# Performance work log

Hardware: AMD Instinct MI355X
Metric: run time of the kernel (lower is better)

Reference implementation:

```python
import jax, jax.numpy as jnp
import numpy as np

D_MODEL = 768
NUM_HEADS = 12
DEPTH = D_MODEL // NUM_HEADS


def setup_inputs() -> dict:
    key = jax.random.key(0)
    ks = jax.random.split(key, 11)
    B, S, D = 2, 2048, D_MODEL
    scale = 1.0 / np.sqrt(D)
    inp = {
        "v": jax.random.normal(ks[0], (B, S, D), jnp.float32),
        "k": jax.random.normal(ks[1], (B, S, D), jnp.float32),
        "q": jax.random.normal(ks[2], (B, S, D), jnp.float32),
        "wq": jax.random.normal(ks[3], (D, D), jnp.float32) * scale,
        "bq": jnp.zeros((D,), jnp.float32),
        "wk": jax.random.normal(ks[4], (D, D), jnp.float32) * scale,
        "bk": jnp.zeros((D,), jnp.float32),
        "wv": jax.random.normal(ks[5], (D, D), jnp.float32) * scale,
        "bv": jnp.zeros((D,), jnp.float32),
        "wo": jax.random.normal(ks[6], (D, D), jnp.float32) * scale,
        "bo": jnp.zeros((D,), jnp.float32),
    }
    return inp


def _split_heads(x):
    # (B, S, D) -> (B, H, S, depth)
    B, S, _ = x.shape
    return x.reshape(B, S, NUM_HEADS, DEPTH).transpose(0, 2, 1, 3)


def reference(v, k, q, wq, bq, wk, bk, wv, bv, wo, bo):
    B, S, D = q.shape
    qh = _split_heads(q @ wq + bq)  # (B,H,S,dh)
    kh = _split_heads(k @ wk + bk)
    vh = _split_heads(v @ wv + bv)
    logits = jnp.einsum("bhqd,bhkd->bhqk", qh, kh) / jnp.sqrt(
        jnp.asarray(DEPTH, qh.dtype)
    )
    attn = jax.nn.softmax(logits, axis=-1)  # (B,H,S,S)
    ctx = jnp.einsum("bhqk,bhkd->bhqd", attn, vh)
    ctx = ctx.transpose(0, 2, 1, 3).reshape(B, S, D)
    return ctx @ wo + bo
```

## Files before the change

kernel.cpp:

```cpp
#include <hip/hip_runtime.h>
#include <hip/hip_bf16.h>
#include <math.h>

typedef __bf16 bf16;
typedef __attribute__((ext_vector_type(8))) __bf16 bf16x8;
typedef __attribute__((ext_vector_type(4))) __bf16 bf16x4v;
typedef __attribute__((ext_vector_type(4))) float f32x4;

#define MFMA16(a, b, c) __builtin_amdgcn_mfma_f32_16x16x32_bf16(a, b, c, 0, 0, 0)

__device__ __forceinline__ void gld16(const bf16* g, bf16* l) {
  __builtin_amdgcn_global_load_lds((const __attribute__((address_space(1))) void*)g,
                                   (__attribute__((address_space(3))) void*)l, 16, 0, 0);
}

__global__ __launch_bounds__(256) void prep(const float* __restrict__ q,
                                            const float* __restrict__ k,
                                            const float* __restrict__ v,
                                            bf16* __restrict__ qb, bf16* __restrict__ kb,
                                            bf16* __restrict__ vb,
                                            const float* __restrict__ w0,
                                            const float* __restrict__ w1,
                                            const float* __restrict__ w2,
                                            const float* __restrict__ w3,
                                            bf16* __restrict__ t0, bf16* __restrict__ t1,
                                            bf16* __restrict__ t2, bf16* __restrict__ t3) {
  const int lin = blockIdx.x;
  if (lin < 4608) {
    const int which = lin / 1536, idx = lin % 1536;
    const float* a = which == 0 ? q : (which == 1 ? k : v);
    bf16* o = which == 0 ? qb : (which == 1 ? kb : vb);
    const size_t i = ((size_t)idx * 256 + threadIdx.x) * 8;
    const float4 f0 = *(const float4*)(a + i);
    const float4 f1 = *(const float4*)(a + i + 4);
    bf16x8 r = {(bf16)f0.x, (bf16)f0.y, (bf16)f0.z, (bf16)f0.w,
                (bf16)f1.x, (bf16)f1.y, (bf16)f1.z, (bf16)f1.w};
    *(bf16x8*)(o + i) = r;
  } else {
    const int w = lin - 4608;
    const int z = w / 576, rem = w % 576;
    const int by = rem / 24, bx = rem % 24;
    const float* W = z == 0 ? w0 : (z == 1 ? w1 : (z == 2 ? w2 : w3));
    bf16* T = z == 0 ? t0 : (z == 1 ? t1 : (z == 2 ? t2 : t3));
    __shared__ float t[32][33];
    const int tx = threadIdx.x & 31, ty = threadIdx.x >> 5;
    const int c0 = bx * 32, r0 = by * 32;
#pragma unroll
    for (int i = 0; i < 4; ++i) {
      const int r = ty + 8 * i;
      t[r][tx] = W[(size_t)(r0 + r) * 768 + c0 + tx];
    }
    __syncthreads();
#pragma unroll
    for (int i = 0; i < 4; ++i) {
      const int r = ty + 8 * i;
      T[(size_t)(c0 + r) * 768 + r0 + tx] = (bf16)t[tx][r];
    }
  }
}

__device__ __forceinline__ void gemm_core(const bf16* __restrict__ A, const bf16* __restrict__ BT,
                                          int row0, int col0, bf16* As, bf16* Bs,
                                          f32x4 acc[4][4]) {
  const int tid = threadIdx.x;
  const int lane = tid & 63, wave = tid >> 6;
  const int m15 = lane & 15, kg = lane >> 4;
  const int wm = wave >> 1, wn = wave & 1;
  const int pr16 = lane & 15;
  const int pk8 = (lane >> 4) * 8;
#pragma unroll
  for (int i = 0; i < 4; ++i)
#pragma unroll
    for (int j = 0; j < 4; ++j) acc[i][j] = f32x4{0.f, 0.f, 0.f, 0.f};

  for (int k0 = 0; k0 < 768; k0 += 32) {
#pragma unroll
    for (int j = 0; j < 2; ++j) {
      const int i = wave * 2 + j;
      gld16(A + (size_t)(row0 + 16 * i + pr16) * 768 + k0 + pk8, As + i * 512);
      gld16(BT + (size_t)(col0 + 16 * i + pr16) * 768 + k0 + pk8, Bs + i * 512);
    }
    __syncthreads();
    bf16x8 af[4], bfr[4];
#pragma unroll
    for (int t = 0; t < 4; ++t)
      af[t] = *(const bf16x8*)(As + (4 * wm + t) * 512 + kg * 128 + m15 * 8);
#pragma unroll
    for (int t = 0; t < 4; ++t)
      bfr[t] = *(const bf16x8*)(Bs + (4 * wn + t) * 512 + kg * 128 + m15 * 8);
#pragma unroll
    for (int mt = 0; mt < 4; ++mt)
#pragma unroll
      for (int nt = 0; nt < 4; ++nt) acc[mt][nt] = MFMA16(af[mt], bfr[nt], acc[mt][nt]);
    __syncthreads();
  }
}

__global__ __launch_bounds__(256, 3) void gemm_qkv(
    const bf16* __restrict__ qb, const bf16* __restrict__ kb, const bf16* __restrict__ vb,
    const bf16* __restrict__ wqT, const bf16* __restrict__ wkT, const bf16* __restrict__ wvT,
    const float* __restrict__ bq, const float* __restrict__ bk, const float* __restrict__ bv,
    bf16* __restrict__ Qh, bf16* __restrict__ Kh, bf16* __restrict__ Vt) {
  __shared__ bf16 As[128 * 32], Bs[128 * 32];
  const bf16 *A, *BT;
  const float* bias;
  bf16* out;
  int mode;
  if (blockIdx.z == 0) { A = qb; BT = wqT; bias = bq; out = Qh; mode = 0; }
  else if (blockIdx.z == 1) { A = kb; BT = wkT; bias = bk; out = Kh; mode = 0; }
  else { A = vb; BT = wvT; bias = bv; out = Vt; mode = 1; }
  const int row0 = blockIdx.y * 128, col0 = blockIdx.x * 128;
  f32x4 acc[4][4];
  gemm_core(A, BT, row0, col0, As, Bs, acc);

  const int lane = threadIdx.x & 63, wave = threadIdx.x >> 6;
  const int m15 = lane & 15, kg = lane >> 4;
  const int wm = wave >> 1, wn = wave & 1;
#pragma unroll
  for (int mt = 0; mt < 4; ++mt) {
#pragma unroll
    for (int nt = 0; nt < 4; ++nt) {
      const int col = col0 + 64 * wn + 16 * nt + m15;
      const float bb = bias[col];
      const int h = col >> 6, d = col & 63;
      const int rowb = row0 + 64 * wm + 16 * mt + kg * 4;
      const int b = rowb >> 11, s0 = rowb & 2047;
      if (mode == 0) {
#pragma unroll
        for (int r = 0; r < 4; ++r)
          out[((size_t)(b * 12 + h) * 2048 + s0 + r) * 64 + d] = (bf16)(acc[mt][nt][r] + bb);
      } else {
        bf16x4v pk;
#pragma unroll
        for (int r = 0; r < 4; ++r) pk[r] = (bf16)(acc[mt][nt][r] + bb);
        *(bf16x4v*)&out[((size_t)(b * 12 + h) * 64 + d) * 2048 + s0] = pk;
      }
    }
  }
}

__global__ __launch_bounds__(256, 3) void gemm_out(const bf16* __restrict__ A,
                                                   const bf16* __restrict__ BT,
                                                   const float* __restrict__ bias,
                                                   float* __restrict__ out) {
  __shared__ bf16 As[64 * 32], Bs[64 * 32];
  const int tid = threadIdx.x;
  const int lane = tid & 63, wave = tid >> 6;
  const int m15 = lane & 15, kg = lane >> 4;
  const int wm = wave >> 1, wn = wave & 1;
  const int row0 = blockIdx.y * 64, col0 = blockIdx.x * 64;
  const int pr16 = lane & 15, pk8 = (lane >> 4) * 8;

  f32x4 acc[2][2];
#pragma unroll
  for (int i = 0; i < 2; ++i)
#pragma unroll
    for (int j = 0; j < 2; ++j) acc[i][j] = f32x4{0.f, 0.f, 0.f, 0.f};

  for (int k0 = 0; k0 < 768; k0 += 32) {
    gld16(A + (size_t)(row0 + 16 * wave + pr16) * 768 + k0 + pk8, As + wave * 512);
    gld16(BT + (size_t)(col0 + 16 * wave + pr16) * 768 + k0 + pk8, Bs + wave * 512);
    __syncthreads();
    bf16x8 af[2], bfr[2];
#pragma unroll
    for (int t = 0; t < 2; ++t)
      af[t] = *(const bf16x8*)(As + (2 * wm + t) * 512 + kg * 128 + m15 * 8);
#pragma unroll
    for (int t = 0; t < 2; ++t)
      bfr[t] = *(const bf16x8*)(Bs + (2 * wn + t) * 512 + kg * 128 + m15 * 8);
#pragma unroll
    for (int mt = 0; mt < 2; ++mt)
#pragma unroll
      for (int nt = 0; nt < 2; ++nt) acc[mt][nt] = MFMA16(af[mt], bfr[nt], acc[mt][nt]);
    __syncthreads();
  }
#pragma unroll
  for (int mt = 0; mt < 2; ++mt) {
#pragma unroll
    for (int nt = 0; nt < 2; ++nt) {
      const int col = col0 + 32 * wn + 16 * nt + m15;
      const float bb = bias[col];
#pragma unroll
      for (int r = 0; r < 4; ++r) {
        const int row = row0 + 32 * wm + 16 * mt + kg * 4 + r;
        out[(size_t)row * 768 + col] = acc[mt][nt][r] + bb;
      }
    }
  }
}

__global__ __launch_bounds__(256, 3) void attn_kernel(const bf16* __restrict__ Q,
                                                      const bf16* __restrict__ K,
                                                      const bf16* __restrict__ VT,
                                                      bf16* __restrict__ ctx) {
  __shared__ __align__(16) char SMEM[33792];

  const int tid = threadIdx.x;
  const int lane = tid & 63, wave = tid >> 6;
  const int m15 = lane & 15, kg = lane >> 4;
  const int lin = blockIdx.x;
  const int bh = lin % 24, rg = lin / 24;
  const size_t hb = (size_t)bh * 2048 * 64;
  const bf16* Qp = Q + hb;
  const bf16* Kp = K + hb;
  const bf16* Vp = VT + hb;
  const int qrow0 = rg * 64;
  bf16* Pw = (bf16*)SMEM + wave * 2560;

  bf16x8 qf[4][2];
#pragma unroll
  for (int rt = 0; rt < 4; ++rt)
#pragma unroll
    for (int ks = 0; ks < 2; ++ks) {
      bf16x8 tv = *(const bf16x8*)&Qp[(size_t)(qrow0 + 16 * rt + m15) * 64 + 32 * ks + kg * 8];
#pragma unroll
      for (int j = 0; j < 8; ++j) tv[j] = (bf16)((float)tv[j] * 0.125f);
      qf[rt][ks] = tv;
    }

  f32x4 o[4][4];
  float lp[4];
#pragma unroll
  for (int rt = 0; rt < 4; ++rt) {
#pragma unroll
    for (int mt = 0; mt < 4; ++mt) o[rt][mt] = f32x4{0.f, 0.f, 0.f, 0.f};
    lp[rt] = 0.f;
  }

  const int kbase = wave * 512;
  for (int c = 0; c < 16; ++c) {
    const int kc = kbase + c * 32;
    bf16x8 kf[2][2];
#pragma unroll
    for (int kt = 0; kt < 2; ++kt)
#pragma unroll
      for (int ks = 0; ks < 2; ++ks)
        kf[kt][ks] = *(const bf16x8*)&Kp[(size_t)(kc + 16 * kt + m15) * 64 + 32 * ks + kg * 8];
    bf16x8 vf[4];
#pragma unroll
    for (int mt = 0; mt < 4; ++mt)
      vf[mt] = *(const bf16x8*)&Vp[(size_t)(16 * mt + m15) * 2048 + kc + kg * 8];
    f32x4 s[2][4];
#pragma unroll
    for (int kt = 0; kt < 2; ++kt)
#pragma unroll
      for (int rt = 0; rt < 4; ++rt) s[kt][rt] = f32x4{0.f, 0.f, 0.f, 0.f};
#pragma unroll
    for (int ks = 0; ks < 2; ++ks)
#pragma unroll
      for (int kt = 0; kt < 2; ++kt)
#pragma unroll
        for (int rt = 0; rt < 4; ++rt) s[kt][rt] = MFMA16(kf[kt][ks], qf[rt][ks], s[kt][rt]);
#pragma unroll
    for (int kt = 0; kt < 2; ++kt)
#pragma unroll
      for (int rt = 0; rt < 4; ++rt) {
        bf16x4v pk;
#pragma unroll
        for (int r = 0; r < 4; ++r) {
          const float pe = __expf(s[kt][rt][r]);
          lp[rt] += pe;
          pk[r] = (bf16)pe;
        }
        *(bf16x4v*)&Pw[rt * 640 + m15 * 40 + 16 * kt + 4 * kg] = pk;
      }
    asm volatile("s_waitcnt lgkmcnt(0)" ::: "memory");
#pragma unroll
    for (int rt = 0; rt < 4; ++rt) {
      const bf16x8 pf = *(const bf16x8*)&Pw[rt * 640 + m15 * 40 + kg * 8];
#pragma unroll
      for (int mt = 0; mt < 4; ++mt) o[rt][mt] = MFMA16(vf[mt], pf, o[rt][mt]);
    }
  }

#pragma unroll
  for (int rt = 0; rt < 4; ++rt) {
    lp[rt] += __shfl_xor(lp[rt], 16);
    lp[rt] += __shfl_xor(lp[rt], 32);
  }

  float* R0 = (float*)SMEM;
  float* R1 = (float*)(SMEM + 16384);
  float* LP = (float*)(SMEM + 32768);
  __syncthreads();
  if (kg == 0) {
#pragma unroll
    for (int rt = 0; rt < 4; ++rt) LP[wave * 64 + rt * 16 + m15] = lp[rt];
  }
  if (wave == 1 || wave == 3) {
    float* R = (wave == 1) ? R0 : R1;
#pragma unroll
    for (int rt = 0; rt < 4; ++rt)
#pragma unroll
      for (int mt = 0; mt < 4; ++mt)
        *(f32x4*)&R[((rt * 4 + mt) * 64 + lane) * 4] = o[rt][mt];
  }
  __syncthreads();
  if (wave == 0 || wave == 2) {
    float* R = (wave == 0) ? R0 : R1;
#pragma unroll
    for (int rt = 0; rt < 4; ++rt)
#pragma unroll
      for (int mt = 0; mt < 4; ++mt) {
        const f32x4 po = *(const f32x4*)&R[((rt * 4 + mt) * 64 + lane) * 4];
#pragma unroll
        for (int j = 0; j < 4; ++j) o[rt][mt][j] += po[j];
      }
  }
  __syncthreads();
  if (wave == 2) {
#pragma unroll
    for (int rt = 0; rt < 4; ++rt)
#pragma unroll
      for (int mt = 0; mt < 4; ++mt)
        *(f32x4*)&R1[((rt * 4 + mt) * 64 + lane) * 4] = o[rt][mt];
  }
  __syncthreads();
  if (wave == 0) {
    const int b = bh / 12, h = bh % 12;
#pragma unroll
    for (int rt = 0; rt < 4; ++rt) {
      const float lsum = LP[0 * 64 + rt * 16 + m15] + LP[1 * 64 + rt * 16 + m15] +
                         LP[2 * 64 + rt * 16 + m15] + LP[3 * 64 + rt * 16 + m15];
      const float inv = 1.0f / lsum;
      const int sr = qrow0 + 16 * rt + m15;
#pragma unroll
      for (int mt = 0; mt < 4; ++mt) {
        const f32x4 po = *(const f32x4*)&R1[((rt * 4 + mt) * 64 + lane) * 4];
        bf16x4v pk;
#pragma unroll
        for (int r = 0; r < 4; ++r) pk[r] = (bf16)((o[rt][mt][r] + po[r]) * inv);
        *(bf16x4v*)&ctx[((size_t)(b * 2048) + sr) * 768 + h * 64 + 16 * mt + 4 * kg] = pk;
      }
    }
  }
}

extern "C" void kernel_launch(void* const* d_in, const int* in_sizes, int n_in,
                              void* d_out, int out_size, void* d_ws, size_t ws_size,
                              hipStream_t stream) {
  const float* v = (const float*)d_in[0];
  const float* k = (const float*)d_in[1];
  const float* q = (const float*)d_in[2];
  const float* wq = (const float*)d_in[3];
  const float* bq = (const float*)d_in[4];
  const float* wk = (const float*)d_in[5];
  const float* bk = (const float*)d_in[6];
  const float* wv = (const float*)d_in[7];
  const float* bv = (const float*)d_in[8];
  const float* wo = (const float*)d_in[9];
  const float* bo = (const float*)d_in[10];

  char* ws = (char*)d_ws;
  const size_t SEG = (size_t)4096 * 768 * sizeof(bf16);
  const size_t WSEG = (size_t)768 * 768 * sizeof(bf16);
  bf16* Qh = (bf16*)(ws + 0 * SEG);
  bf16* Kh = (bf16*)(ws + 1 * SEG);
  bf16* Vt = (bf16*)(ws + 2 * SEG);
  bf16* qb = (bf16*)(ws + 3 * SEG);
  bf16* kb = (bf16*)(ws + 4 * SEG);
  bf16* vb = (bf16*)(ws + 5 * SEG);
  bf16* ctx = qb;
  bf16* wqT = (bf16*)(ws + 6 * SEG);
  bf16* wkT = (bf16*)(ws + 6 * SEG + WSEG);
  bf16* wvT = (bf16*)(ws + 6 * SEG + 2 * WSEG);
  bf16* woT = (bf16*)(ws + 6 * SEG + 3 * WSEG);

  prep<<<dim3(6912), 256, 0, stream>>>(q, k, v, qb, kb, vb, wq, wk, wv, wo,
                                       wqT, wkT, wvT, woT);
  gemm_qkv<<<dim3(6, 32, 3), 256, 0, stream>>>(qb, kb, vb, wqT, wkT, wvT, bq, bk, bv,
                                               Qh, Kh, Vt);
  attn_kernel<<<dim3(768), 256, 0, stream>>>(Qh, Kh, Vt, ctx);
  gemm_out<<<dim3(12, 64), 256, 0, stream>>>(ctx, woT, bo, (float*)d_out);
}
```

Measured before the change: 217.9 us.

## Retile projection GEMMs to 128x96/64x96 with BK=64 and tune attention exp path

```diff
diff --git a/kernel.cpp b/kernel.cpp
--- a/kernel.cpp
+++ b/kernel.cpp
@@ -59,73 +59,70 @@
   }
 }
 
-__device__ __forceinline__ void gemm_core(const bf16* __restrict__ A, const bf16* __restrict__ BT,
-                                          int row0, int col0, bf16* As, bf16* Bs,
-                                          f32x4 acc[4][4]) {
-  const int tid = threadIdx.x;
-  const int lane = tid & 63, wave = tid >> 6;
-  const int m15 = lane & 15, kg = lane >> 4;
-  const int wm = wave >> 1, wn = wave & 1;
-  const int pr16 = lane & 15;
-  const int pk8 = (lane >> 4) * 8;
-#pragma unroll
-  for (int i = 0; i < 4; ++i)
-#pragma unroll
-    for (int j = 0; j < 4; ++j) acc[i][j] = f32x4{0.f, 0.f, 0.f, 0.f};
-
-  for (int k0 = 0; k0 < 768; k0 += 32) {
-#pragma unroll
-    for (int j = 0; j < 2; ++j) {
-      const int i = wave * 2 + j;
-      gld16(A + (size_t)(row0 + 16 * i + pr16) * 768 + k0 + pk8, As + i * 512);
-      gld16(BT + (size_t)(col0 + 16 * i + pr16) * 768 + k0 + pk8, Bs + i * 512);
-    }
-    __syncthreads();
-    bf16x8 af[4], bfr[4];
-#pragma unroll
-    for (int t = 0; t < 4; ++t)
-      af[t] = *(const bf16x8*)(As + (4 * wm + t) * 512 + kg * 128 + m15 * 8);
-#pragma unroll
-    for (int t = 0; t < 4; ++t)
-      bfr[t] = *(const bf16x8*)(Bs + (4 * wn + t) * 512 + kg * 128 + m15 * 8);
-#pragma unroll
-    for (int mt = 0; mt < 4; ++mt)
-#pragma unroll
-      for (int nt = 0; nt < 4; ++nt) acc[mt][nt] = MFMA16(af[mt], bfr[nt], acc[mt][nt]);
-    __syncthreads();
-  }
-}
-
 __global__ __launch_bounds__(256, 3) void gemm_qkv(
     const bf16* __restrict__ qb, const bf16* __restrict__ kb, const bf16* __restrict__ vb,
     const bf16* __restrict__ wqT, const bf16* __restrict__ wkT, const bf16* __restrict__ wvT,
     const float* __restrict__ bq, const float* __restrict__ bk, const float* __restrict__ bv,
     bf16* __restrict__ Qh, bf16* __restrict__ Kh, bf16* __restrict__ Vt) {
-  __shared__ bf16 As[128 * 32], Bs[128 * 32];
+  __shared__ bf16 As[128 * 64];
+  __shared__ bf16 Bs[96 * 64];
   const bf16 *A, *BT;
   const float* bias;
-  bf16* out;
   int mode;
-  if (blockIdx.z == 0) { A = qb; BT = wqT; bias = bq; out = Qh; mode = 0; }
-  else if (blockIdx.z == 1) { A = kb; BT = wkT; bias = bk; out = Kh; mode = 0; }
-  else { A = vb; BT = wvT; bias = bv; out = Vt; mode = 1; }
-  const int row0 = blockIdx.y * 128, col0 = blockIdx.x * 128;
-  f32x4 acc[4][4];
-  gemm_core(A, BT, row0, col0, As, Bs, acc);
-
-  const int lane = threadIdx.x & 63, wave = threadIdx.x >> 6;
+  if (blockIdx.z == 0) { A = qb; BT = wqT; bias = bq; mode = 0; }
+  else if (blockIdx.z == 1) { A = kb; BT = wkT; bias = bk; mode = 0; }
+  else { A = vb; BT = wvT; bias = bv; mode = 1; }
+  const int row0 = blockIdx.y * 128, col0 = blockIdx.x * 96;
+
+  const int tid = threadIdx.x;
+  const int lane = tid & 63, wave = tid >> 6;
   const int m15 = lane & 15, kg = lane >> 4;
   const int wm = wave >> 1, wn = wave & 1;
+  const int srow = ((tid >> 7) << 4) + (tid & 15);
+  const int sk = ((tid >> 4) & 7) * 8;
+
+  f32x4 acc[4][3];
+#pragma unroll
+  for (int i = 0; i < 4; ++i)
+#pragma unroll
+    for (int j = 0; j < 3; ++j) acc[i][j] = f32x4{0.f, 0.f, 0.f, 0.f};
+
+  for (int k0 = 0; k0 < 768; k0 += 64) {
+#pragma unroll
+    for (int j = 0; j < 4; ++j)
+      gld16(A + (size_t)(row0 + j * 32 + srow) * 768 + k0 + sk, As + j * 2048 + tid * 8);
+#pragma unroll
+    for (int j = 0; j < 3; ++j)
+      gld16(BT + (size_t)(col0 + j * 32 + srow) * 768 + k0 + sk, Bs + j * 2048 + tid * 8);
+    __syncthreads();
+#pragma unroll
+    for (int kh = 0; kh < 2; ++kh) {
+      bf16x8 af[4], bfr[3];
+#pragma unroll
+      for (int t = 0; t < 4; ++t)
+        af[t] = *(const bf16x8*)(As + (4 * wm + t) * 1024 + (kh * 4 + kg) * 128 + m15 * 8);
+#pragma unroll
+      for (int t = 0; t < 3; ++t)
+        bfr[t] = *(const bf16x8*)(Bs + (3 * wn + t) * 1024 + (kh * 4 + kg) * 128 + m15 * 8);
+#pragma unroll
+      for (int mt = 0; mt < 4; ++mt)
+#pragma unroll
+        for (int nt = 0; nt < 3; ++nt) acc[mt][nt] = MFMA16(af[mt], bfr[nt], acc[mt][nt]);
+    }
+    __syncthreads();
+  }
+
 #pragma unroll
   for (int mt = 0; mt < 4; ++mt) {
 #pragma unroll
-    for (int nt = 0; nt < 4; ++nt) {
-      const int col = col0 + 64 * wn + 16 * nt + m15;
+    for (int nt = 0; nt < 3; ++nt) {
+      const int col = col0 + 48 * wn + 16 * nt + m15;
       const float bb = bias[col];
       const int h = col >> 6, d = col & 63;
       const int rowb = row0 + 64 * wm + 16 * mt + kg * 4;
       const int b = rowb >> 11, s0 = rowb & 2047;
       if (mode == 0) {
+        bf16* out = (blockIdx.z == 0) ? Qh : Kh;
 #pragma unroll
         for (int r = 0; r < 4; ++r)
           out[((size_t)(b * 12 + h) * 2048 + s0 + r) * 64 + d] = (bf16)(acc[mt][nt][r] + bb);
@@ -133,7 +130,7 @@
         bf16x4v pk;
 #pragma unroll
         for (int r = 0; r < 4; ++r) pk[r] = (bf16)(acc[mt][nt][r] + bb);
-        *(bf16x4v*)&out[((size_t)(b * 12 + h) * 64 + d) * 2048 + s0] = pk;
+        *(bf16x4v*)&Vt[((size_t)(b * 12 + h) * 64 + d) * 2048 + s0] = pk;
       }
     }
   }
@@ -143,42 +140,50 @@
                                                    const bf16* __restrict__ BT,
                                                    const float* __restrict__ bias,
                                                    float* __restrict__ out) {
-  __shared__ bf16 As[64 * 32], Bs[64 * 32];
+  __shared__ bf16 As[64 * 64], Bs[96 * 64];
   const int tid = threadIdx.x;
   const int lane = tid & 63, wave = tid >> 6;
   const int m15 = lane & 15, kg = lane >> 4;
   const int wm = wave >> 1, wn = wave & 1;
-  const int row0 = blockIdx.y * 64, col0 = blockIdx.x * 64;
-  const int pr16 = lane & 15, pk8 = (lane >> 4) * 8;
-
-  f32x4 acc[2][2];
+  const int row0 = blockIdx.y * 64, col0 = blockIdx.x * 96;
+  const int srow = ((tid >> 7) << 4) + (tid & 15);
+  const int sk = ((tid >> 4) & 7) * 8;
+
+  f32x4 acc[2][3];
 #pragma unroll
   for (int i = 0; i < 2; ++i)
 #pragma unroll
-    for (int j = 0; j < 2; ++j) acc[i][j] = f32x4{0.f, 0.f, 0.f, 0.f};
-
-  for (int k0 = 0; k0 < 768; k0 += 32) {
-    gld16(A + (size_t)(row0 + 16 * wave + pr16) * 768 + k0 + pk8, As + wave * 512);
-    gld16(BT + (size_t)(col0 + 16 * wave + pr16) * 768 + k0 + pk8, Bs + wave * 512);
-    __syncthreads();
-    bf16x8 af[2], bfr[2];
-#pragma unroll
-    for (int t = 0; t < 2; ++t)
-      af[t] = *(const bf16x8*)(As + (2 * wm + t) * 512 + kg * 128 + m15 * 8);
-#pragma unroll
-    for (int t = 0; t < 2; ++t)
-      bfr[t] = *(const bf16x8*)(Bs + (2 * wn + t) * 512 + kg * 128 + m15 * 8);
-#pragma unroll
-    for (int mt = 0; mt < 2; ++mt)
-#pragma unroll
-      for (int nt = 0; nt < 2; ++nt) acc[mt][nt] = MFMA16(af[mt], bfr[nt], acc[mt][nt]);
+    for (int j = 0; j < 3; ++j) acc[i][j] = f32x4{0.f, 0.f, 0.f, 0.f};
+
+  for (int k0 = 0; k0 < 768; k0 += 64) {
+#pragma unroll
+    for (int j = 0; j < 2; ++j)
+      gld16(A + (size_t)(row0 + j * 32 + srow) * 768 + k0 + sk, As + j * 2048 + tid * 8);
+#pragma unroll
+    for (int j = 0; j < 3; ++j)
+      gld16(BT + (size_t)(col0 + j * 32 + srow) * 768 + k0 + sk, Bs + j * 2048 + tid * 8);
+    __syncthreads();
+#pragma unroll
+    for (int kh = 0; kh < 2; ++kh) {
+      bf16x8 af[2], bfr[3];
+#pragma unroll
+      for (int t = 0; t < 2; ++t)
+        af[t] = *(const bf16x8*)(As + (2 * wm + t) * 1024 + (kh * 4 + kg) * 128 + m15 * 8);
+#pragma unroll
+      for (int t = 0; t < 3; ++t)
+        bfr[t] = *(const bf16x8*)(Bs + (3 * wn + t) * 1024 + (kh * 4 + kg) * 128 + m15 * 8);
+#pragma unroll
+      for (int mt = 0; mt < 2; ++mt)
+#pragma unroll
+        for (int nt = 0; nt < 3; ++nt) acc[mt][nt] = MFMA16(af[mt], bfr[nt], acc[mt][nt]);
+    }
     __syncthreads();
   }
 #pragma unroll
   for (int mt = 0; mt < 2; ++mt) {
 #pragma unroll
-    for (int nt = 0; nt < 2; ++nt) {
-      const int col = col0 + 32 * wn + 16 * nt + m15;
+    for (int nt = 0; nt < 3; ++nt) {
+      const int col = col0 + 48 * wn + 16 * nt + m15;
       const float bb = bias[col];
 #pragma unroll
       for (int r = 0; r < 4; ++r) {
@@ -193,7 +198,7 @@
                                                       const bf16* __restrict__ K,
                                                       const bf16* __restrict__ VT,
                                                       bf16* __restrict__ ctx) {
-  __shared__ __align__(16) char SMEM[33792];
+  __shared__ __align__(16) char SMEM[36864];
 
   const int tid = threadIdx.x;
   const int lane = tid & 63, wave = tid >> 6;
@@ -205,7 +210,7 @@
   const bf16* Kp = K + hb;
   const bf16* Vp = VT + hb;
   const int qrow0 = rg * 64;
-  bf16* Pw = (bf16*)SMEM + wave * 2560;
+  bf16* Pw = (bf16*)SMEM + wave * 4608;
 
   bf16x8 qf[4][2];
 #pragma unroll
@@ -214,7 +219,7 @@
     for (int ks = 0; ks < 2; ++ks) {
       bf16x8 tv = *(const bf16x8*)&Qp[(size_t)(qrow0 + 16 * rt + m15) * 64 + 32 * ks + kg * 8];
 #pragma unroll
-      for (int j = 0; j < 8; ++j) tv[j] = (bf16)((float)tv[j] * 0.125f);
+      for (int j = 0; j < 8; ++j) tv[j] = (bf16)((float)tv[j] * 0.18033688011f);
       qf[rt][ks] = tv;
     }
 
@@ -228,6 +233,7 @@
   }
 
   const int kbase = wave * 512;
+#pragma unroll 2
   for (int c = 0; c < 16; ++c) {
     const int kc = kbase + c * 32;
     bf16x8 kf[2][2];
@@ -258,16 +264,15 @@
         bf16x4v pk;
 #pragma unroll
         for (int r = 0; r < 4; ++r) {
-          const float pe = __expf(s[kt][rt][r]);
+          const float pe = __builtin_exp2f(s[kt][rt][r]);
           lp[rt] += pe;
           pk[r] = (bf16)pe;
         }
-        *(bf16x4v*)&Pw[rt * 640 + m15 * 40 + 16 * kt + 4 * kg] = pk;
-      }
-    asm volatile("s_waitcnt lgkmcnt(0)" ::: "memory");
+        *(bf16x4v*)&Pw[rt * 1152 + m15 * 72 + 16 * kt + 4 * kg] = pk;
+      }
 #pragma unroll
     for (int rt = 0; rt < 4; ++rt) {
-      const bf16x8 pf = *(const bf16x8*)&Pw[rt * 640 + m15 * 40 + kg * 8];
+      const bf16x8 pf = *(const bf16x8*)&Pw[rt * 1152 + m15 * 72 + kg * 8];
 #pragma unroll
       for (int mt = 0; mt < 4; ++mt) o[rt][mt] = MFMA16(vf[mt], pf, o[rt][mt]);
     }
@@ -368,8 +373,8 @@
 
   prep<<<dim3(6912), 256, 0, stream>>>(q, k, v, qb, kb, vb, wq, wk, wv, wo,
                                        wqT, wkT, wvT, woT);
-  gemm_qkv<<<dim3(6, 32, 3), 256, 0, stream>>>(qb, kb, vb, wqT, wkT, wvT, bq, bk, bv,
+  gemm_qkv<<<dim3(8, 32, 3), 256, 0, stream>>>(qb, kb, vb, wqT, wkT, wvT, bq, bk, bv,
                                                Qh, Kh, Vt);
   attn_kernel<<<dim3(768), 256, 0, stream>>>(Qh, Kh, Vt, ctx);
-  gemm_out<<<dim3(12, 64), 256, 0, stream>>>(ctx, woT, bo, (float*)d_out);
-}
+  gemm_out<<<dim3(8, 64), 256, 0, stream>>>(ctx, woT, bo, (float*)d_out);
+}
```

Result: slower. 274.1 us (+25.8%).
